# Kernel tuning notes

Hardware: AMD Instinct MI355X
Metric: run time of the kernel (lower is better)

The kernel has to match this reference:

```python
import jax, jax.numpy as jnp
import numpy as np
from jax import lax


def squash(x, axis=-1):
    sq = jnp.sum(x * x, axis=axis, keepdims=True)
    n = jnp.sqrt(sq)
    return jnp.tanh(n) * x / (n + 1e-8)


def setup_inputs() -> dict:
    key = jax.random.key(0)
    ks = jax.random.split(key, 12)
    B = 2048
    x = jax.random.normal(ks[0], (B, 64, 22, 22), dtype=jnp.float32)
    conv1_w = 0.02 * jax.random.normal(ks[1], (256, 64, 9, 9), dtype=jnp.float32)
    conv1_b = jnp.zeros((256,), jnp.float32)
    pc_w = 0.02 * jax.random.normal(ks[2], (48, 256, 8, 8), dtype=jnp.float32)  # out_channels*num_conv_units=8*6
    pc_b = jnp.zeros((48,), jnp.float32)
    W_digit = 0.01 * jax.random.normal(ks[3], (1, 2, 96, 16, 8), dtype=jnp.float32)  # (1,out_caps,in_caps,out_dim,in_dim)
    dec_w1 = 0.05 * jax.random.normal(ks[4], (512, 32), dtype=jnp.float32)  # in = out_dim*num_classes = 16*2
    dec_b1 = jnp.zeros((512,), jnp.float32)
    dec_w2 = 0.03 * jax.random.normal(ks[5], (1024, 512), dtype=jnp.float32)
    dec_b2 = jnp.zeros((1024,), jnp.float32)
    dec_w3 = 0.03 * jax.random.normal(ks[6], (256, 1024), dtype=jnp.float32)  # fusion_dim=256
    dec_b3 = jnp.zeros((256,), jnp.float32)
    return dict(x=x, conv1_w=conv1_w, conv1_b=conv1_b, pc_w=pc_w, pc_b=pc_b,
                W_digit=W_digit, dec_w1=dec_w1, dec_b1=dec_b1, dec_w2=dec_w2,
                dec_b2=dec_b2, dec_w3=dec_w3, dec_b3=dec_b3)


def reference(x, conv1_w, conv1_b, pc_w, pc_b, W_digit,
              dec_w1, dec_b1, dec_w2, dec_b2, dec_w3, dec_b3):
    DN = ('NCHW', 'OIHW', 'NCHW')
    NUM_ROUTING = 2
    OUT_CAPS = 2
    # conv1 + relu: (B,64,22,22) -> (B,256,14,14)
    out = lax.conv_general_dilated(x, conv1_w, (1, 1), 'VALID', dimension_numbers=DN)
    out = jax.nn.relu(out + conv1_b[None, :, None, None])
    # primary caps conv: -> (B,48,4,4)
    pc = lax.conv_general_dilated(out, pc_w, (2, 2), 'VALID', dimension_numbers=DN)
    pc = pc + pc_b[None, :, None, None]
    B = pc.shape[0]
    u = squash(pc.reshape(B, -1, 8), axis=-1)  # (B, 96, 8)
    # u_hat: W (out_caps,in_caps,out_dim,in_dim) x u (B,in_caps,in_dim) -> (B,out_caps,in_caps,out_dim)
    u_hat = jnp.einsum('oidk,bik->boid', W_digit[0], u)
    tmp = lax.stop_gradient(u_hat)
    b = jnp.zeros((B, OUT_CAPS, 96, 1), u_hat.dtype)
    for _ in range(NUM_ROUTING - 1):
        c = jax.nn.softmax(b, axis=1)                     # over out_caps
        v = squash(jnp.sum(c * tmp, axis=2))              # (B,out_caps,out_dim)
        b = jnp.einsum('boid,bod->boi', tmp, v)[..., None]
    c = jax.nn.softmax(b, axis=1)
    v = squash(jnp.sum(c * u_hat, axis=2))                # (B,out_caps,out_dim)
    logits = jnp.linalg.norm(v, axis=-1)                  # (B,out_caps)
    pred = jax.nn.one_hot(jnp.argmax(logits, axis=1), OUT_CAPS, dtype=v.dtype)  # (B,out_caps)
    h = (v * pred[:, :, None]).reshape(B, -1)             # (B, out_caps*out_dim)
    h = jax.nn.relu(h @ dec_w1.T + dec_b1)
    h = jax.nn.relu(h @ dec_w2.T + dec_b2)
    recon = jax.nn.sigmoid(h @ dec_w3.T + dec_b3)
    return logits, recon
```

## Files before the change

### kernel.cpp

```cpp
#include <hip/hip_runtime.h>
#include <cstdint>
#include <cstddef>

typedef short short8 __attribute__((ext_vector_type(8)));
typedef short short4v __attribute__((ext_vector_type(4)));
typedef float f32x16 __attribute__((ext_vector_type(16)));
typedef float f32x4 __attribute__((ext_vector_type(4)));

__device__ inline unsigned short bf16_rne(float x) {
    unsigned u = __float_as_uint(x);
    unsigned r = u + 0x7FFFu + ((u >> 16) & 1u);
    return (unsigned short)(r >> 16);
}
__device__ inline float bf16_to_f(unsigned short h) {
    return __uint_as_float(((unsigned)h) << 16);
}

__global__ void reorder_wf_kernel(const float* __restrict__ w, unsigned short* __restrict__ wf) {
    int idx = blockIdx.x * 256 + threadIdx.x;
    if (idx >= 324 * 8 * 64 * 8) return;
    int j   = idx & 7;
    int l   = (idx >> 3) & 63;
    int nc  = (idx >> 9) & 7;
    int ksg = idx >> 12;
    int cc  = ksg / 81;
    int tap = ksg - cc * 81;
    int ci  = cc * 16 + ((l >> 5) << 3) + j;
    int co  = nc * 32 + (l & 31);
    float v = w[(co * 64 + ci) * 81 + tap];
    unsigned short hi = bf16_rne(v);
    unsigned short lo = bf16_rne(v - bf16_to_f(hi));
    size_t base = ((size_t)(ksg * 8 + nc)) * 1024;
    wf[base + l * 8 + j]       = hi;
    wf[base + 512 + l * 8 + j] = lo;
}

__global__ void reorder_pcwf_kernel(const float* __restrict__ w, unsigned short* __restrict__ wf) {
    int idx = blockIdx.x * 256 + threadIdx.x;
    if (idx >= 1572864) return;
    int j     = idx & 7;
    int l     = (idx >> 3) & 63;
    int plane = (idx >> 9) & 1;
    int rest  = idx >> 10;
    int ct    = rest % 3;
    int rest2 = rest / 3;
    int tap   = rest2 & 63;
    int cc    = rest2 >> 6;
    int co = ct * 16 + (l & 15);
    int ci = cc * 32 + ((l >> 4) << 3) + j;
    float v = w[((size_t)co * 256 + ci) * 64 + tap];
    unsigned short hi = bf16_rne(v);
    unsigned short out = plane ? bf16_rne(v - bf16_to_f(hi)) : hi;
    wf[idx] = out;
}

#define RS 40

__global__ __launch_bounds__(512, 1) void conv1_mfma_kernel(
    const float* __restrict__ x, const unsigned short* __restrict__ wf,
    const float* __restrict__ b1, float* __restrict__ c1o, int c0)
{
    __shared__ __align__(16) unsigned short Xs[484 * RS];
    const int t  = threadIdx.x;
    const int l  = t & 63;
    const int w  = t >> 6;
    const int il = blockIdx.x;
    const int bg = c0 + il;
    const int lane31 = l & 31;
    const int kg = l >> 5;
    const int co = w * 32 + lane31;
    const float bias = b1[co];

    int am[7];
#pragma unroll
    for (int mt = 0; mt < 7; ++mt) {
        int p  = mt * 32 + lane31;
        int pp = (p < 196) ? p : 0;
        int oh = pp / 14, ow = pp - oh * 14;
        am[mt] = (oh * 22 + ow) * RS + kg * 8;
    }
    const char* wfb = (const char*)wf;
    const int boff = w * 2048 + l * 16;

    const int sidx = t >> 2;
    const int sblk = t & 3;

    f32x16 acc[7];
#pragma unroll
    for (int mt = 0; mt < 7; ++mt) acc[mt] = (f32x16)(0.f);

#pragma unroll
    for (int r = 0; r < 4; ++r) {
        int s = sidx + r * 128;
        if (s < 484) {
            short4v hv, lv;
#pragma unroll
            for (int e = 0; e < 4; ++e) {
                float xv = x[((size_t)bg * 64 + sblk * 4 + e) * 484 + s];
                unsigned short hi = bf16_rne(xv);
                hv[e] = (short)hi;
                lv[e] = (short)bf16_rne(xv - bf16_to_f(hi));
            }
            *(short4v*)(Xs + s * RS + sblk * 4)      = hv;
            *(short4v*)(Xs + s * RS + 16 + sblk * 4) = lv;
        }
    }
    __syncthreads();

    for (int cc = 0; cc < 4; ++cc) {
        float vx[4][4];
        if (cc < 3) {
#pragma unroll
            for (int r = 0; r < 4; ++r) {
                int s = sidx + r * 128;
                if (s < 484) {
#pragma unroll
                    for (int e = 0; e < 4; ++e)
                        vx[r][e] = x[((size_t)bg * 64 + (cc + 1) * 16 + sblk * 4 + e) * 484 + s];
                }
            }
        }

        const int ksgb = cc * 81;
        short8 bh0 = *(const short8*)(wfb + (size_t)ksgb * 16384 + boff);
        short8 bl0 = *(const short8*)(wfb + (size_t)ksgb * 16384 + 1024 + boff);

        for (int tap = 0; tap < 81; ++tap) {
            int kn = ksgb + tap + 1; if (kn > 323) kn = 323;
            short8 bh1 = *(const short8*)(wfb + (size_t)kn * 16384 + boff);
            short8 bl1 = *(const short8*)(wfb + (size_t)kn * 16384 + 1024 + boff);

            const int kh = tap / 9, kw = tap - kh * 9;
            const int toff = (kh * 22 + kw) * RS;
#pragma unroll
            for (int mt = 0; mt < 7; ++mt) {
                const int a = am[mt] + toff;
                short8 Ah = *(const short8*)(Xs + a);
                short8 Al = *(const short8*)(Xs + a + 16);
                acc[mt] = __builtin_amdgcn_mfma_f32_32x32x16_bf16(Ah, bh0, acc[mt], 0, 0, 0);
                acc[mt] = __builtin_amdgcn_mfma_f32_32x32x16_bf16(Ah, bl0, acc[mt], 0, 0, 0);
                acc[mt] = __builtin_amdgcn_mfma_f32_32x32x16_bf16(Al, bh0, acc[mt], 0, 0, 0);
                acc[mt] = __builtin_amdgcn_mfma_f32_32x32x16_bf16(Al, bl0, acc[mt], 0, 0, 0);
            }
            bh0 = bh1; bl0 = bl1;
        }

        if (cc < 3) {
            __syncthreads();
#pragma unroll
            for (int r = 0; r < 4; ++r) {
                int s = sidx + r * 128;
                if (s < 484) {
                    short4v hv, lv;
#pragma unroll
                    for (int e = 0; e < 4; ++e) {
                        float xv = vx[r][e];
                        unsigned short hi = bf16_rne(xv);
                        hv[e] = (short)hi;
                        lv[e] = (short)bf16_rne(xv - bf16_to_f(hi));
                    }
                    *(short4v*)(Xs + s * RS + sblk * 4)      = hv;
                    *(short4v*)(Xs + s * RS + 16 + sblk * 4) = lv;
                }
            }
            __syncthreads();
        }
    }

#pragma unroll
    for (int mt = 0; mt < 7; ++mt) {
#pragma unroll
        for (int r = 0; r < 16; ++r) {
            int p = mt * 32 + (r & 3) + ((r >> 2) << 3) + kg * 4;
            if (p < 196) {
                float v = acc[mt][r] + bias;
                c1o[((size_t)il * 196 + p) * 256 + co] = fmaxf(v, 0.f);
            }
        }
    }
}

#define PC_RS 36

__global__ __launch_bounds__(256, 2) void pc_mfma_kernel(
    const float* __restrict__ c1o, const unsigned short* __restrict__ pcwf,
    const float* __restrict__ pcb, float* __restrict__ pco)
{
    __shared__ unsigned short Xh[196 * PC_RS];
    __shared__ unsigned short Xl[196 * PC_RS];
    const int t  = threadIdx.x;
    const int l  = t & 63;
    const int w  = t >> 6;
    const int il = blockIdx.x;
    const int pos = l & 15;
    const int kg  = l >> 4;
    const int oh = pos >> 2, ow = pos & 3;
    const char* wb = (const char*)pcwf;

    f32x4 acc0 = (f32x4)(0.f), acc1 = (f32x4)(0.f), acc2 = (f32x4)(0.f);

    for (int cc = 0; cc < 8; ++cc) {
        __syncthreads();
        for (int q = t; q < 1568; q += 256) {
            int p  = q >> 3;
            int c4 = (q & 7) << 2;
            const float4 v = *(const float4*)(c1o + ((size_t)il * 196 + p) * 256 + cc * 32 + c4);
            short4v hv, lv;
#pragma unroll
            for (int e = 0; e < 4; ++e) {
                float xv = ((const float*)&v)[e];
                unsigned short hi = bf16_rne(xv);
                hv[e] = (short)hi;
                lv[e] = (short)bf16_rne(xv - bf16_to_f(hi));
            }
            *(short4v*)(Xh + p * PC_RS + c4) = hv;
            *(short4v*)(Xl + p * PC_RS + c4) = lv;
        }
        __syncthreads();

        short8 Bh0[3], Bl0[3], Bh1[3], Bl1[3];
        {
            const char* bp = wb + ((size_t)(cc * 64 + w) * 6) * 1024 + l * 16;
#pragma unroll
            for (int ct = 0; ct < 3; ++ct) {
                Bh0[ct] = *(const short8*)(bp + ct * 2048);
                Bl0[ct] = *(const short8*)(bp + ct * 2048 + 1024);
            }
        }
        for (int tt = 0; tt < 16; ++tt) {
            const int tap = tt * 4 + w;
            const int tapn = (tt == 15) ? tap : (tap + 4);
            const char* bpn = wb + ((size_t)(cc * 64 + tapn) * 6) * 1024 + l * 16;
#pragma unroll
            for (int ct = 0; ct < 3; ++ct) {
                Bh1[ct] = *(const short8*)(bpn + ct * 2048);
                Bl1[ct] = *(const short8*)(bpn + ct * 2048 + 1024);
            }
            const int kh = tap >> 3, kw = tap & 7;
            const int pix = (2 * oh + kh) * 14 + (2 * ow + kw);
            const int a = pix * PC_RS + kg * 8;
            short4v h0 = *(const short4v*)(Xh + a);
            short4v h1 = *(const short4v*)(Xh + a + 4);
            short4v q0 = *(const short4v*)(Xl + a);
            short4v q1 = *(const short4v*)(Xl + a + 4);
            short8 Ah = __builtin_shufflevector(h0, h1, 0, 1, 2, 3, 4, 5, 6, 7);
            short8 Al = __builtin_shufflevector(q0, q1, 0, 1, 2, 3, 4, 5, 6, 7);

            acc0 = __builtin_amdgcn_mfma_f32_16x16x32_bf16(Ah, Bh0[0], acc0, 0, 0, 0);
            acc0 = __builtin_amdgcn_mfma_f32_16x16x32_bf16(Ah, Bl0[0], acc0, 0, 0, 0);
            acc0 = __builtin_amdgcn_mfma_f32_16x16x32_bf16(Al, Bh0[0], acc0, 0, 0, 0);
            acc0 = __builtin_amdgcn_mfma_f32_16x16x32_bf16(Al, Bl0[0], acc0, 0, 0, 0);
            acc1 = __builtin_amdgcn_mfma_f32_16x16x32_bf16(Ah, Bh0[1], acc1, 0, 0, 0);
            acc1 = __builtin_amdgcn_mfma_f32_16x16x32_bf16(Ah, Bl0[1], acc1, 0, 0, 0);
            acc1 = __builtin_amdgcn_mfma_f32_16x16x32_bf16(Al, Bh0[1], acc1, 0, 0, 0);
            acc1 = __builtin_amdgcn_mfma_f32_16x16x32_bf16(Al, Bl0[1], acc1, 0, 0, 0);
            acc2 = __builtin_amdgcn_mfma_f32_16x16x32_bf16(Ah, Bh0[2], acc2, 0, 0, 0);
            acc2 = __builtin_amdgcn_mfma_f32_16x16x32_bf16(Ah, Bl0[2], acc2, 0, 0, 0);
            acc2 = __builtin_amdgcn_mfma_f32_16x16x32_bf16(Al, Bh0[2], acc2, 0, 0, 0);
            acc2 = __builtin_amdgcn_mfma_f32_16x16x32_bf16(Al, Bl0[2], acc2, 0, 0, 0);
#pragma unroll
            for (int ct = 0; ct < 3; ++ct) { Bh0[ct] = Bh1[ct]; Bl0[ct] = Bl1[ct]; }
        }
    }

    __syncthreads();
    float* R = (float*)Xh;
#pragma unroll
    for (int ct = 0; ct < 3; ++ct) {
        f32x4 a = (ct == 0) ? acc0 : (ct == 1) ? acc1 : acc2;
#pragma unroll
        for (int r = 0; r < 4; ++r)
            R[(((w * 3 + ct) * 64) + l) * 4 + r] = a[r];
    }
    __syncthreads();
    for (int idx = t; idx < 768; idx += 256) {
        int pp = idx & 15, co = idx >> 4;
        int ct = co >> 4, col = co & 15;
        int lane = ((pp >> 2) << 4) | col, reg = pp & 3;
        float s = 0.f;
#pragma unroll
        for (int w4 = 0; w4 < 4; ++w4)
            s += R[(((w4 * 3 + ct) * 64) + lane) * 4 + reg];
        pco[(size_t)il * 768 + idx] = s + pcb[co];
    }
}

__global__ __launch_bounds__(64) void caps_kernel(
    const float* __restrict__ pco, const float* __restrict__ Wd,
    float* __restrict__ logits_out, float* __restrict__ hbuf, int c0) {
    __shared__ float u_s[96][8];
    __shared__ float uh[2][96][16];
    __shared__ float vv[2][16];
    __shared__ float cc2[2][96];
    __shared__ float lg_s[2];
    const int t = threadIdx.x;
    const int il = blockIdx.x;

    for (int cap = t; cap < 96; cap += 64) {
        float xr[8];
        float n2 = 0.f;
#pragma unroll
        for (int k = 0; k < 8; ++k) {
            xr[k] = pco[(size_t)il * 768 + cap * 8 + k];
            n2 = fmaf(xr[k], xr[k], n2);
        }
        float nr = sqrtf(n2);
        float sc = tanhf(nr) / (nr + 1e-8f);
#pragma unroll
        for (int k = 0; k < 8; ++k) u_s[cap][k] = xr[k] * sc;
    }
    __syncthreads();
    for (int j = t; j < 3072; j += 64) {
        int d = j & 15;
        int oi = j >> 4;
        int i = oi % 96;
        int o = oi / 96;
        float acc = 0.f;
#pragma unroll
        for (int k = 0; k < 8; ++k)
            acc = fmaf(Wd[(size_t)j * 8 + k], u_s[i][k], acc);
        uh[o][i][d] = acc;
    }
    __syncthreads();
    const int o = t >> 4, d = t & 15;
    if (t < 32) {
        float s = 0.f;
        for (int i = 0; i < 96; ++i) s += 0.5f * uh[o][i][d];
        float n2 = s * s;
        n2 += __shfl_xor(n2, 1); n2 += __shfl_xor(n2, 2);
        n2 += __shfl_xor(n2, 4); n2 += __shfl_xor(n2, 8);
        float nr = sqrtf(n2);
        vv[o][d] = tanhf(nr) * s / (nr + 1e-8f);
    }
    __syncthreads();
    for (int j = t; j < 192; j += 64) {
        int oo = j / 96, ii = j - oo * 96;
        float bsum = 0.f;
#pragma unroll
        for (int dd = 0; dd < 16; ++dd)
            bsum = fmaf(uh[oo][ii][dd], vv[oo][dd], bsum);
        cc2[oo][ii] = bsum;
    }
    __syncthreads();
    for (int ii = t; ii < 96; ii += 64) {
        float b0 = cc2[0][ii], b1v = cc2[1][ii];
        float m = fmaxf(b0, b1v);
        float e0 = expf(b0 - m), e1 = expf(b1v - m);
        float inv = 1.f / (e0 + e1);
        cc2[0][ii] = e0 * inv;
        cc2[1][ii] = e1 * inv;
    }
    __syncthreads();
    if (t < 32) {
        float s = 0.f;
        for (int i = 0; i < 96; ++i) s = fmaf(cc2[o][i], uh[o][i][d], s);
        float n2 = s * s;
        n2 += __shfl_xor(n2, 1); n2 += __shfl_xor(n2, 2);
        n2 += __shfl_xor(n2, 4); n2 += __shfl_xor(n2, 8);
        float nr = sqrtf(n2);
        float v = tanhf(nr) * s / (nr + 1e-8f);
        float n2v = v * v;
        n2v += __shfl_xor(n2v, 1); n2v += __shfl_xor(n2v, 2);
        n2v += __shfl_xor(n2v, 4); n2v += __shfl_xor(n2v, 8);
        vv[o][d] = v;
        if (d == 0) {
            float lg = sqrtf(n2v);
            lg_s[o] = lg;
            logits_out[(size_t)(c0 + il) * 2 + o] = lg;
        }
    }
    __syncthreads();
    if (t < 32) {
        int ostar = (lg_s[1] > lg_s[0]) ? 1 : 0;
        hbuf[(size_t)il * 32 + t] = (o == ostar) ? vv[o][d] : 0.f;
    }
}

__global__ __launch_bounds__(256) void fc_kernel(
    const float* __restrict__ in, const float* __restrict__ W,
    const float* __restrict__ bias, float* __restrict__ out,
    int M, int N, int K, int act) {
    __shared__ float As[64][33];
    __shared__ float Bs[64][33];
    const int t = threadIdx.x;
    const int m0 = blockIdx.x * 64, n0 = blockIdx.y * 64;
    const int tn = t & 15, tm = t >> 4;
    float acc[4][4];
#pragma unroll
    for (int i = 0; i < 4; ++i)
#pragma unroll
        for (int j = 0; j < 4; ++j) acc[i][j] = 0.f;
    const int rr = t >> 2, c8 = (t & 3) * 8;
    for (int kc = 0; kc < K; kc += 32) {
        __syncthreads();
        const int mrow = m0 + rr;
#pragma unroll
        for (int q = 0; q < 8; ++q) {
            As[rr][c8 + q] = (mrow < M) ? in[(size_t)mrow * K + kc + c8 + q] : 0.f;
            Bs[rr][c8 + q] = W[(size_t)(n0 + rr) * K + kc + c8 + q];
        }
        __syncthreads();
#pragma unroll
        for (int k = 0; k < 32; ++k) {
            float av[4], bv[4];
#pragma unroll
            for (int i = 0; i < 4; ++i) av[i] = As[tm * 4 + i][k];
#pragma unroll
            for (int j = 0; j < 4; ++j) bv[j] = Bs[tn * 4 + j][k];
#pragma unroll
            for (int i = 0; i < 4; ++i)
#pragma unroll
                for (int j = 0; j < 4; ++j) acc[i][j] = fmaf(av[i], bv[j], acc[i][j]);
        }
    }
#pragma unroll
    for (int i = 0; i < 4; ++i) {
        int m = m0 + tm * 4 + i;
        if (m < M) {
#pragma unroll
            for (int j = 0; j < 4; ++j) {
                int nn = n0 + tn * 4 + j;
                float v = acc[i][j] + bias[nn];
                if (act == 0) v = fmaxf(v, 0.f);
                else v = 1.f / (1.f + expf(-v));
                out[(size_t)m * N + nn] = v;
            }
        }
    }
}

extern "C" void kernel_launch(void* const* d_in, const int* in_sizes, int n_in,
                              void* d_out, int out_size, void* d_ws, size_t ws_size,
                              hipStream_t stream) {
    const float* x    = (const float*)d_in[0];
    const float* w1   = (const float*)d_in[1];
    const float* b1   = (const float*)d_in[2];
    const float* pcw  = (const float*)d_in[3];
    const float* pcb  = (const float*)d_in[4];
    const float* Wd   = (const float*)d_in[5];
    const float* dw1  = (const float*)d_in[6];
    const float* db1  = (const float*)d_in[7];
    const float* dw2  = (const float*)d_in[8];
    const float* db2  = (const float*)d_in[9];
    const float* dw3  = (const float*)d_in[10];
    const float* db3  = (const float*)d_in[11];
    float* out = (float*)d_out;

    const int B = 2048;
    float* ws = (float*)d_ws;
    unsigned short* wf = (unsigned short*)ws;
    unsigned short* pcwf = (unsigned short*)(ws + 1327104);
    float* dyn  = ws + 1327104 + 786432;

    const long long base_floats = 1327104LL + 786432LL;
    const long long per_img = 50176 + 768 + 32 + 512 + 1024;
    long long avail = (long long)(ws_size / 4) - base_floats;
    int CH;
    if (avail < per_img) CH = 1;
    else CH = (int)(avail / per_img);
    if (CH > B) CH = B;

    reorder_wf_kernel<<<(324 * 8 * 64 * 8 + 255) / 256, 256, 0, stream>>>(w1, wf);
    reorder_pcwf_kernel<<<(1572864 + 255) / 256, 256, 0, stream>>>(pcw, pcwf);

    float* c1o  = dyn;
    float* pco  = c1o  + (size_t)CH * 50176;
    float* hbuf = pco  + (size_t)CH * 768;
    float* h1   = hbuf + (size_t)CH * 32;
    float* h2   = h1   + (size_t)CH * 512;

    for (int c0 = 0; c0 < B; c0 += CH) {
        int n = B - c0; if (n > CH) n = CH;
        conv1_mfma_kernel<<<n, 512, 0, stream>>>(x, wf, b1, c1o, c0);
        pc_mfma_kernel<<<n, 256, 0, stream>>>(c1o, pcwf, pcb, pco);
        caps_kernel<<<n, 64, 0, stream>>>(pco, Wd, out, hbuf, c0);
        fc_kernel<<<dim3((n + 63) / 64, 8),  256, 0, stream>>>(hbuf, dw1, db1, h1, n, 512, 32, 0);
        fc_kernel<<<dim3((n + 63) / 64, 16), 256, 0, stream>>>(h1,   dw2, db2, h2, n, 1024, 512, 0);
        fc_kernel<<<dim3((n + 63) / 64, 4),  256, 0, stream>>>(h2,   dw3, db3, out + 4096 + (size_t)c0 * 256, n, 256, 1024, 1);
    }
}
```

Before: 3.807 ms.

## Retile conv1 waves to split output rows and share A fragments across two channel tiles

Conv1 work is re-split across waves. Before, each wave owned 32 output channels across all 7 row tiles. Now four waves take 4 row tiles and four take 3, each covering 64 channels, so each LDS A fragment feeds two MFMA column tiles. The MFMA sequence is also interleaved across independent accumulators instead of chaining four MFMAs on one accumulator. The trade-off is twice the weight loads per wave, more accumulator registers, and an uneven 4-vs-3 split that puts more MFMAs on the slowest wave's path.

```diff
diff --git a/kernel.cpp b/kernel.cpp
--- a/kernel.cpp
+++ b/kernel.cpp
@@ -56,38 +56,40 @@
 
 #define RS 40
 
-__global__ __launch_bounds__(512, 1) void conv1_mfma_kernel(
-    const float* __restrict__ x, const unsigned short* __restrict__ wf,
-    const float* __restrict__ b1, float* __restrict__ c1o, int c0)
+template<int MTC>
+__device__ __forceinline__ void conv1_body(
+    unsigned short* Xs, const float* __restrict__ x,
+    const unsigned short* __restrict__ wf, const float* __restrict__ b1,
+    float* __restrict__ c1o, int bg, int il, int t, int mtbase)
 {
-    __shared__ __align__(16) unsigned short Xs[484 * RS];
-    const int t  = threadIdx.x;
-    const int l  = t & 63;
-    const int w  = t >> 6;
-    const int il = blockIdx.x;
-    const int bg = c0 + il;
+    const int l = t & 63;
+    const int w = t >> 6;
+    const int ncg = w & 3;
     const int lane31 = l & 31;
     const int kg = l >> 5;
-    const int co = w * 32 + lane31;
-    const float bias = b1[co];
-
-    int am[7];
-#pragma unroll
-    for (int mt = 0; mt < 7; ++mt) {
-        int p  = mt * 32 + lane31;
+    const int c0a = (ncg * 2) * 32 + lane31;
+    const int c1a = c0a + 32;
+    const float biasA = b1[c0a];
+    const float biasB = b1[c1a];
+
+    int am[MTC];
+#pragma unroll
+    for (int i = 0; i < MTC; ++i) {
+        int p = (mtbase + i) * 32 + lane31;
         int pp = (p < 196) ? p : 0;
         int oh = pp / 14, ow = pp - oh * 14;
-        am[mt] = (oh * 22 + ow) * RS + kg * 8;
+        am[i] = (oh * 22 + ow) * RS + kg * 8;
     }
     const char* wfb = (const char*)wf;
-    const int boff = w * 2048 + l * 16;
+    const int boffA = (ncg * 2) * 2048 + l * 16;
+    const int boffB = boffA + 2048;
 
     const int sidx = t >> 2;
     const int sblk = t & 3;
 
-    f32x16 acc[7];
-#pragma unroll
-    for (int mt = 0; mt < 7; ++mt) acc[mt] = (f32x16)(0.f);
+    f32x16 acc[MTC][2];
+#pragma unroll
+    for (int i = 0; i < MTC; ++i) { acc[i][0] = (f32x16)(0.f); acc[i][1] = (f32x16)(0.f); }
 
 #pragma unroll
     for (int r = 0; r < 4; ++r) {
@@ -122,27 +124,47 @@
         }
 
         const int ksgb = cc * 81;
-        short8 bh0 = *(const short8*)(wfb + (size_t)ksgb * 16384 + boff);
-        short8 bl0 = *(const short8*)(wfb + (size_t)ksgb * 16384 + 1024 + boff);
+        const char* bp0 = wfb + (size_t)ksgb * 16384;
+        short8 bhA0 = *(const short8*)(bp0 + boffA);
+        short8 blA0 = *(const short8*)(bp0 + 1024 + boffA);
+        short8 bhB0 = *(const short8*)(bp0 + boffB);
+        short8 blB0 = *(const short8*)(bp0 + 1024 + boffB);
 
         for (int tap = 0; tap < 81; ++tap) {
             int kn = ksgb + tap + 1; if (kn > 323) kn = 323;
-            short8 bh1 = *(const short8*)(wfb + (size_t)kn * 16384 + boff);
-            short8 bl1 = *(const short8*)(wfb + (size_t)kn * 16384 + 1024 + boff);
+            const char* bpn = wfb + (size_t)kn * 16384;
+            short8 bhA1 = *(const short8*)(bpn + boffA);
+            short8 blA1 = *(const short8*)(bpn + 1024 + boffA);
+            short8 bhB1 = *(const short8*)(bpn + boffB);
+            short8 blB1 = *(const short8*)(bpn + 1024 + boffB);
 
             const int kh = tap / 9, kw = tap - kh * 9;
             const int toff = (kh * 22 + kw) * RS;
-#pragma unroll
-            for (int mt = 0; mt < 7; ++mt) {
-                const int a = am[mt] + toff;
-                short8 Ah = *(const short8*)(Xs + a);
-                short8 Al = *(const short8*)(Xs + a + 16);
-                acc[mt] = __builtin_amdgcn_mfma_f32_32x32x16_bf16(Ah, bh0, acc[mt], 0, 0, 0);
-                acc[mt] = __builtin_amdgcn_mfma_f32_32x32x16_bf16(Ah, bl0, acc[mt], 0, 0, 0);
-                acc[mt] = __builtin_amdgcn_mfma_f32_32x32x16_bf16(Al, bh0, acc[mt], 0, 0, 0);
-                acc[mt] = __builtin_amdgcn_mfma_f32_32x32x16_bf16(Al, bl0, acc[mt], 0, 0, 0);
-            }
-            bh0 = bh1; bl0 = bl1;
+            short8 Ah[MTC], Al[MTC];
+#pragma unroll
+            for (int i = 0; i < MTC; ++i) {
+                const int a = am[i] + toff;
+                Ah[i] = *(const short8*)(Xs + a);
+                Al[i] = *(const short8*)(Xs + a + 16);
+            }
+#pragma unroll
+            for (int i = 0; i < MTC; ++i) acc[i][0] = __builtin_amdgcn_mfma_f32_32x32x16_bf16(Ah[i], bhA0, acc[i][0], 0, 0, 0);
+#pragma unroll
+            for (int i = 0; i < MTC; ++i) acc[i][1] = __builtin_amdgcn_mfma_f32_32x32x16_bf16(Ah[i], bhB0, acc[i][1], 0, 0, 0);
+#pragma unroll
+            for (int i = 0; i < MTC; ++i) acc[i][0] = __builtin_amdgcn_mfma_f32_32x32x16_bf16(Al[i], bhA0, acc[i][0], 0, 0, 0);
+#pragma unroll
+            for (int i = 0; i < MTC; ++i) acc[i][1] = __builtin_amdgcn_mfma_f32_32x32x16_bf16(Al[i], bhB0, acc[i][1], 0, 0, 0);
+#pragma unroll
+            for (int i = 0; i < MTC; ++i) acc[i][0] = __builtin_amdgcn_mfma_f32_32x32x16_bf16(Ah[i], blA0, acc[i][0], 0, 0, 0);
+#pragma unroll
+            for (int i = 0; i < MTC; ++i) acc[i][1] = __builtin_amdgcn_mfma_f32_32x32x16_bf16(Ah[i], blB0, acc[i][1], 0, 0, 0);
+#pragma unroll
+            for (int i = 0; i < MTC; ++i) acc[i][0] = __builtin_amdgcn_mfma_f32_32x32x16_bf16(Al[i], blA0, acc[i][0], 0, 0, 0);
+#pragma unroll
+            for (int i = 0; i < MTC; ++i) acc[i][1] = __builtin_amdgcn_mfma_f32_32x32x16_bf16(Al[i], blB0, acc[i][1], 0, 0, 0);
+
+            bhA0 = bhA1; blA0 = blA1; bhB0 = bhB1; blB0 = blB1;
         }
 
         if (cc < 3) {
@@ -168,16 +190,29 @@
     }
 
 #pragma unroll
-    for (int mt = 0; mt < 7; ++mt) {
+    for (int i = 0; i < MTC; ++i) {
 #pragma unroll
         for (int r = 0; r < 16; ++r) {
-            int p = mt * 32 + (r & 3) + ((r >> 2) << 3) + kg * 4;
+            int p = (mtbase + i) * 32 + (r & 3) + ((r >> 2) << 3) + kg * 4;
             if (p < 196) {
-                float v = acc[mt][r] + bias;
-                c1o[((size_t)il * 196 + p) * 256 + co] = fmaxf(v, 0.f);
-            }
-        }
-    }
+                size_t row = ((size_t)il * 196 + p) * 256;
+                c1o[row + c0a] = fmaxf(acc[i][0][r] + biasA, 0.f);
+                c1o[row + c1a] = fmaxf(acc[i][1][r] + biasB, 0.f);
+            }
+        }
+    }
+}
+
+__global__ __launch_bounds__(512, 1) void conv1_mfma_kernel(
+    const float* __restrict__ x, const unsigned short* __restrict__ wf,
+    const float* __restrict__ b1, float* __restrict__ c1o, int c0)
+{
+    __shared__ __align__(16) unsigned short Xs[484 * RS];
+    const int t  = threadIdx.x;
+    const int il = blockIdx.x;
+    const int bg = c0 + il;
+    if ((t >> 6) < 4) conv1_body<4>(Xs, x, wf, b1, c1o, bg, il, t, 0);
+    else              conv1_body<3>(Xs, x, wf, b1, c1o, bg, il, t, 4);
 }
 
 #define PC_RS 36
```

Measured after the change: 4.135 ms. 1.09x slower.
